# Kernel optimization log

Measured on AMD Instinct MI355X. Metric: run time of the kernel, lower is better.

The kernel has to match this reference:

```python
import jax, jax.numpy as jnp
import numpy as np
import math

S, E, D, H = 4096, 512, 64, 8  # sentence_length, imbd_size, hidden_size, num_heads


def setup_inputs() -> dict:
    key = jax.random.key(0)
    k1, k2, k3, k4, k5 = jax.random.split(key, 5)
    return {
        "X": jax.random.normal(k1, (S, E), dtype=jnp.float32),
        "W_q": jax.random.uniform(k2, (H, E, D), dtype=jnp.float32),
        "W_k": jax.random.uniform(k3, (H, E, D), dtype=jnp.float32),
        "W_v": jax.random.uniform(k4, (H, E, D), dtype=jnp.float32),
        "W_0": jax.random.uniform(k5, (E, D), dtype=jnp.float32),
    }


def reference(X, W_q, W_k, W_v, W_0):
    # Per-head projections: X [S,E] broadcast across heads -> [H,S,D]
    q = jnp.einsum('se,hed->hsd', X, W_q)
    k = jnp.einsum('se,hed->hsd', X, W_k)
    v = jnp.einsum('se,hed->hsd', X, W_v)
    # Scaled scores [H,S,S]; softmax over keys (last axis), no mask
    scores = jnp.einsum('hsd,htd->hst', q, k) / math.sqrt(D)
    attn = jax.nn.softmax(scores, axis=-1)
    r3 = jnp.einsum('hst,htd->hsd', attn, v)  # [H,S,D]
    # Concat heads: permute to [S,H,D] -> [S,H*D], then output proj [E,D]
    Z = r3.transpose(1, 0, 2).reshape(S, H * D) @ W_0  # [S,D]
    return Z
```

## Files before the change

kernel.cpp:

```cpp
#include <hip/hip_runtime.h>
#include <hip/hip_bf16.h>

#define S_LEN 4096
#define E_DIM 512
#define D_DIM 64
#define H_NUM 8
#define KSPLIT 4
#define NKT ((S_LEN / KSPLIT) / 64)
#define QSCALE 0.18033688011112042f

typedef short bf16x8 __attribute__((ext_vector_type(8)));
typedef float f32x4 __attribute__((ext_vector_type(4)));
typedef unsigned short u16x8 __attribute__((ext_vector_type(8)));
typedef unsigned short u16x4 __attribute__((ext_vector_type(4)));

__device__ inline unsigned short f2bf(float x) {
    union { float f; unsigned u; } v; v.f = x;
    unsigned r = v.u + 0x7FFFu + ((v.u >> 16) & 1u);
    return (unsigned short)(r >> 16);
}
__device__ inline float bf2f(unsigned short b) {
    union { unsigned u; float f; } v; v.u = ((unsigned)b) << 16;
    return v.f;
}
__device__ inline f32x4 mfma16(bf16x8 a, bf16x8 b, f32x4 c) {
    return __builtin_amdgcn_mfma_f32_16x16x32_bf16(a, b, c, 0, 0, 0);
}
__device__ inline void gl_lds16(const void* g, void* l) {
    __builtin_amdgcn_global_load_lds(
        (const __attribute__((address_space(1))) void*)g,
        (__attribute__((address_space(3))) void*)l, 16, 0, 0);
}
__device__ inline unsigned cvtpk(float a, float b) {
    unsigned r;
    asm volatile("v_cvt_pk_bf16_f32 %0, %1, %2" : "=v"(r) : "v"(a), "v"(b));
    return r;
}

__global__ __launch_bounds__(256) void prepass_x(
    const float* __restrict__ X, unsigned short* __restrict__ Xhi,
    unsigned short* __restrict__ Xlo)
{
    int i = (blockIdx.x * 256 + threadIdx.x) * 4;
    float4 v = *(const float4*)&X[i];
    float a[4] = {v.x, v.y, v.z, v.w};
    u16x4 hv, lv;
#pragma unroll
    for (int j = 0; j < 4; ++j) {
        unsigned short hb = f2bf(a[j]);
        hv[j] = hb;
        lv[j] = f2bf(a[j] - bf2f(hb));
    }
    *(u16x4*)&Xhi[i] = hv;
    *(u16x4*)&Xlo[i] = lv;
}

__global__ __launch_bounds__(256) void prepass_w(
    const float* __restrict__ Wq, const float* __restrict__ Wk,
    const float* __restrict__ Wv, unsigned short* __restrict__ WT)
{
    int z = blockIdx.y;
    const float* W = (z == 0) ? Wq : (z == 1) ? Wk : Wv;
    int idx = blockIdx.x * 256 + threadIdx.x;
    int n = idx >> 7;
    int e = (idx & 127) * 4;
    int hh = n >> 6, d = n & 63;
    unsigned short* Whi = WT + (size_t)z * 2 * 262144;
    unsigned short* Wlo = Whi + 262144;
    u16x4 hv, lv;
#pragma unroll
    for (int j = 0; j < 4; ++j) {
        float v = W[((size_t)hh * E_DIM + e + j) * D_DIM + d];
        unsigned short hb = f2bf(v);
        hv[j] = hb;
        lv[j] = f2bf(v - bf2f(hb));
    }
    *(u16x4*)&Whi[(size_t)n * E_DIM + e] = hv;
    *(u16x4*)&Wlo[(size_t)n * E_DIM + e] = lv;
}

__global__ __launch_bounds__(256) void proj_kernel(
    const unsigned short* __restrict__ Xhi, const unsigned short* __restrict__ Xlo,
    const unsigned short* __restrict__ WT,
    unsigned short* __restrict__ Qhi, unsigned short* __restrict__ Qlo,
    unsigned short* __restrict__ Khi, unsigned short* __restrict__ Klo,
    unsigned short* __restrict__ Vb)
{
    __shared__ __align__(16) unsigned short XhS[128 * 64];
    __shared__ __align__(16) unsigned short XlS[128 * 64];
    __shared__ __align__(16) unsigned short WhS[128 * 64];
    __shared__ __align__(16) unsigned short WlS[128 * 64];

    const int s0 = blockIdx.x * 128, n0 = blockIdx.y * 128, z = blockIdx.z;
    const unsigned short* Wh_g = WT + (size_t)z * 524288;
    const unsigned short* Wl_g = Wh_g + 262144;

    const int tid = threadIdx.x, lane = tid & 63, w = tid >> 6;
    const int l15 = lane & 15, lhi = lane >> 4;
    const int wr = w >> 1, wc = w & 1;

    const int chunk = lane & 7;
    size_t aoff[4], boff[4];
    int ldso[4];
#pragma unroll
    for (int i = 0; i < 4; ++i) {
        int r = w * 32 + i * 8 + (lane >> 3);
        int swz = (chunk * 16) ^ ((r & 7) << 4);
        aoff[i] = ((size_t)(s0 + r)) * 1024 + swz;
        boff[i] = ((size_t)(n0 + r)) * 1024 + swz;
        ldso[i] = (w * 32 + i * 8) * 128;
    }

    f32x4 acc[4][4];
#pragma unroll
    for (int a = 0; a < 4; ++a)
#pragma unroll
        for (int b = 0; b < 4; ++b) acc[a][b] = (f32x4){0.f, 0.f, 0.f, 0.f};

    for (int kb = 0; kb < E_DIM; kb += 64) {
        __syncthreads();
#pragma unroll
        for (int i = 0; i < 4; ++i) {
            size_t ab = aoff[i] + kb * 2;
            size_t bb = boff[i] + kb * 2;
            gl_lds16((const char*)Xhi + ab, (char*)XhS + ldso[i]);
            gl_lds16((const char*)Xlo + ab, (char*)XlS + ldso[i]);
            gl_lds16((const char*)Wh_g + bb, (char*)WhS + ldso[i]);
            gl_lds16((const char*)Wl_g + bb, (char*)WlS + ldso[i]);
        }
        __syncthreads();

#pragma unroll
        for (int kc = 0; kc < 2; ++kc) {
            int cb = kc * 64 + lhi * 16;
            bf16x8 ah[4], al[4], bh[4], bl[4];
#pragma unroll
            for (int rt = 0; rt < 4; ++rt) {
                int row = wr * 64 + rt * 16 + l15;
                int ad = row * 128 + (cb ^ ((row & 7) << 4));
                ah[rt] = *(const bf16x8*)((const char*)XhS + ad);
                al[rt] = *(const bf16x8*)((const char*)XlS + ad);
            }
#pragma unroll
            for (int nt = 0; nt < 4; ++nt) {
                int n = wc * 64 + nt * 16 + l15;
                int bd = n * 128 + (cb ^ ((n & 7) << 4));
                bh[nt] = *(const bf16x8*)((const char*)WhS + bd);
                bl[nt] = *(const bf16x8*)((const char*)WlS + bd);
            }
#pragma unroll
            for (int rt = 0; rt < 4; ++rt)
#pragma unroll
                for (int nt = 0; nt < 4; ++nt) {
                    acc[rt][nt] = mfma16(ah[rt], bh[nt], acc[rt][nt]);
                    acc[rt][nt] = mfma16(ah[rt], bl[nt], acc[rt][nt]);
                    acc[rt][nt] = mfma16(al[rt], bh[nt], acc[rt][nt]);
                }
        }
    }

#pragma unroll
    for (int rt = 0; rt < 4; ++rt)
#pragma unroll
        for (int nt = 0; nt < 4; ++nt) {
            int n = n0 + wc * 64 + nt * 16 + l15;
            int hh = n >> 6, d = n & 63;
#pragma unroll
            for (int j = 0; j < 4; ++j) {
                int s = s0 + wr * 64 + rt * 16 + lhi * 4 + j;
                float val = acc[rt][nt][j];
                size_t o = ((size_t)hh * S_LEN + s) * D_DIM + d;
                if (z == 0) {
                    val *= QSCALE;
                    unsigned short hb = f2bf(val);
                    Qhi[o] = hb;
                    Qlo[o] = f2bf(val - bf2f(hb));
                } else if (z == 1) {
                    unsigned short hb = f2bf(val);
                    Khi[o] = hb;
                    Klo[o] = f2bf(val - bf2f(hb));
                } else {
                    Vb[o] = f2bf(val);
                }
            }
        }
}

__global__ __launch_bounds__(256) void pack_vt(
    const unsigned short* __restrict__ Vb, unsigned short* __restrict__ Vt)
{
    __shared__ unsigned short T[64][72];
    int h = blockIdx.y, sblk = blockIdx.x * 64;
    int t = threadIdx.x;
#pragma unroll
    for (int p = 0; p < 2; ++p) {
        int slot = t + 256 * p;
        int s = slot >> 3, c = slot & 7;
        u16x8 v = *(const u16x8*)&Vb[((size_t)h * S_LEN + sblk + s) * D_DIM + c * 8];
#pragma unroll
        for (int j = 0; j < 8; ++j) T[c * 8 + j][s] = v[j];
    }
    __syncthreads();
#pragma unroll
    for (int p = 0; p < 2; ++p) {
        int slot = t + 256 * p;
        int d = slot >> 3, c = slot & 7;
        u16x8 v;
#pragma unroll
        for (int j = 0; j < 8; ++j) v[j] = T[d][c * 8 + j];
        *(u16x8*)&Vt[((size_t)(h * D_DIM + d)) * S_LEN + sblk + c * 8] = v;
    }
}

__global__ __launch_bounds__(256) void flash_kernel(
    const unsigned short* __restrict__ Qhi, const unsigned short* __restrict__ Qlo,
    const unsigned short* __restrict__ Khi_g, const unsigned short* __restrict__ Klo_g,
    const unsigned short* __restrict__ Vt_g,
    unsigned short* __restrict__ Part, float2* __restrict__ ML)
{
    __shared__ __align__(16) unsigned short KhiS[64 * 64];
    __shared__ __align__(16) unsigned short KloS[64 * 64];
    __shared__ __align__(16) unsigned short VtS[64 * 64];
    __shared__ __align__(16) unsigned short PS[4][16 * 64];

    const int h  = blockIdx.y;
    const int ks = blockIdx.z;
    const int q0 = blockIdx.x * 64;
    const int tid  = threadIdx.x;
    const int lane = tid & 63;
    const int w    = tid >> 6;
    const int l15  = lane & 15;
    const int lhi  = lane >> 4;

    const int qrow = q0 + w * 16 + l15;
    bf16x8 qh[2], ql[2];
#pragma unroll
    for (int c = 0; c < 2; ++c) {
        size_t off = ((size_t)(h * S_LEN + qrow)) * D_DIM + lhi * 8 + 32 * c;
        qh[c] = *(const bf16x8*)&Qhi[off];
        ql[c] = *(const bf16x8*)&Qlo[off];
    }

    const char *pKh[2], *pKl[2], *pV[2];
    int ldsd[2];
    {
        const int chunk = lane & 7;
#pragma unroll
        for (int i = 0; i < 2; ++i) {
            int r = w * 16 + i * 8 + (lane >> 3);
            int swz = (chunk * 16) ^ ((r & 7) << 4);
            size_t kb = ((size_t)(h * S_LEN + ks * (S_LEN / KSPLIT) + r)) * 128 + swz;
            pKh[i] = (const char*)Khi_g + kb;
            pKl[i] = (const char*)Klo_g + kb;
            size_t vb = ((size_t)(h * D_DIM + r) * S_LEN + ks * (S_LEN / KSPLIT)) * 2 + swz;
            pV[i] = (const char*)Vt_g + vb;
            ldsd[i] = (w * 16 + i * 8) * 128;
        }
    }

    f32x4 acc_o[4];
#pragma unroll
    for (int nt = 0; nt < 4; ++nt) acc_o[nt] = (f32x4){0.f, 0.f, 0.f, 0.f};
    float m2 = -1e30f, lsum = 0.f;

    unsigned short* pw = &PS[w][0];

    for (int kt = 0; kt < NKT; ++kt) {
        __syncthreads();
#pragma unroll
        for (int i = 0; i < 2; ++i) {
            gl_lds16(pKh[i], (char*)KhiS + ldsd[i]);
            gl_lds16(pKl[i], (char*)KloS + ldsd[i]);
            gl_lds16(pV[i],  (char*)VtS  + ldsd[i]);
            pKh[i] += 8192; pKl[i] += 8192; pV[i] += 128;
        }
        __syncthreads();

        f32x4 sacc[4];
#pragma unroll
        for (int nt = 0; nt < 4; ++nt) sacc[nt] = (f32x4){0.f, 0.f, 0.f, 0.f};
#pragma unroll
        for (int c = 0; c < 2; ++c) {
            int colb = (lhi * 8 + 32 * c) * 2;
#pragma unroll
            for (int nt = 0; nt < 4; ++nt) {
                int key = l15 + 16 * nt;
                int lo = key * 128 + (((colb >> 4) ^ (key & 7)) << 4);
                bf16x8 kh = *(const bf16x8*)((const char*)KhiS + lo);
                bf16x8 kl = *(const bf16x8*)((const char*)KloS + lo);
                sacc[nt] = mfma16(kh, qh[c], sacc[nt]);
                sacc[nt] = mfma16(kl, qh[c], sacc[nt]);
                sacc[nt] = mfma16(kh, ql[c], sacc[nt]);
            }
        }

        float mx0 = fmaxf(fmaxf(sacc[0][0], sacc[0][1]), fmaxf(sacc[0][2], sacc[0][3]));
        float mx1 = fmaxf(fmaxf(sacc[1][0], sacc[1][1]), fmaxf(sacc[1][2], sacc[1][3]));
        float mx2 = fmaxf(fmaxf(sacc[2][0], sacc[2][1]), fmaxf(sacc[2][2], sacc[2][3]));
        float mx3 = fmaxf(fmaxf(sacc[3][0], sacc[3][1]), fmaxf(sacc[3][2], sacc[3][3]));
        float vm = fmaxf(fmaxf(mx0, mx1), fmaxf(mx2, mx3));
        vm = fmaxf(vm, __shfl_xor(vm, 16));
        vm = fmaxf(vm, __shfl_xor(vm, 32));

        if (!__all(vm <= m2 + 8.f)) {
            float mnew = fmaxf(m2, vm);
            float sc = exp2f(m2 - mnew);
            m2 = mnew;
            lsum *= sc;
            float scj[4];
#pragma unroll
            for (int j = 0; j < 4; ++j) scj[j] = __shfl(sc, lhi * 4 + j);
#pragma unroll
            for (int nt = 0; nt < 4; ++nt)
#pragma unroll
                for (int j = 0; j < 4; ++j) acc_o[nt][j] *= scj[j];
        }

        float sum = 0.f;
#pragma unroll
        for (int nt = 0; nt < 4; ++nt) {
            float e0 = exp2f(sacc[nt][0] - m2);
            float e1 = exp2f(sacc[nt][1] - m2);
            float e2 = exp2f(sacc[nt][2] - m2);
            float e3 = exp2f(sacc[nt][3] - m2);
            sum += (e0 + e1) + (e2 + e3);
            int colb = 32 * nt + 8 * lhi;
            int adr = l15 * 128 + ((((colb >> 4)) ^ (l15 & 7)) << 4) + (colb & 15);
            uint2 pk = make_uint2(cvtpk(e0, e1), cvtpk(e2, e3));
            *(uint2*)((char*)pw + adr) = pk;
        }
        sum += __shfl_xor(sum, 16);
        sum += __shfl_xor(sum, 32);
        lsum += sum;

#pragma unroll
        for (int c = 0; c < 2; ++c) {
            int colb = (lhi * 8 + 32 * c) * 2;
            int loA = l15 * 128 + (((colb >> 4) ^ (l15 & 7)) << 4);
            bf16x8 pa = *(const bf16x8*)((const char*)pw + loA);
#pragma unroll
            for (int nt = 0; nt < 4; ++nt) {
                int d = l15 + 16 * nt;
                int loB = d * 128 + (((colb >> 4) ^ (d & 7)) << 4);
                bf16x8 vb = *(const bf16x8*)((const char*)VtS + loB);
                acc_o[nt] = mfma16(pa, vb, acc_o[nt]);
            }
        }
    }

    if (lane < 16) {
        ML[(size_t)(ks * H_NUM + h) * S_LEN + q0 + w * 16 + l15] =
            make_float2(m2, lsum);
    }
    unsigned short* PT = Part + ((size_t)(ks * H_NUM + h)) * S_LEN * D_DIM;
#pragma unroll
    for (int r = 0; r < 4; ++r) {
        float lr = __shfl(lsum, lhi * 4 + r);
        float inv = 1.f / lr;
        int s = q0 + w * 16 + lhi * 4 + r;
#pragma unroll
        for (int nt = 0; nt < 4; ++nt)
            PT[(size_t)s * D_DIM + l15 + 16 * nt] = f2bf(acc_o[nt][r] * inv);
    }
}

__global__ __launch_bounds__(256) void cw_kernel(
    const float2* __restrict__ ML, float4* __restrict__ CW)
{
    int i = blockIdx.x * 256 + threadIdx.x;
    float2 a[KSPLIT];
    float m = -1e30f;
#pragma unroll
    for (int k = 0; k < KSPLIT; ++k) {
        a[k] = ML[(size_t)k * H_NUM * S_LEN + i];
        m = fmaxf(m, a[k].x);
    }
    float wk[KSPLIT], wsum = 0.f;
#pragma unroll
    for (int k = 0; k < KSPLIT; ++k) {
        wk[k] = exp2f(a[k].x - m) * a[k].y;
        wsum += wk[k];
    }
    float inv = 1.f / wsum;
    CW[i] = make_float4(wk[0] * inv, wk[1] * inv, wk[2] * inv, wk[3] * inv);
}

__global__ __launch_bounds__(256) void zout_kernel(
    const unsigned short* __restrict__ Part, const float4* __restrict__ CW,
    const float* __restrict__ W0, float* __restrict__ Z)
{
    __shared__ __align__(16) float Rs[32][64];
    __shared__ __align__(16) float Ws[32][64];

    const size_t PSZ = (size_t)H_NUM * S_LEN * D_DIM;
    const int s0 = blockIdx.x * 64;
    const int tid = threadIdx.x;
    const int tx = tid & 15;
    const int ty = tid >> 4;

    float acc[4][4];
#pragma unroll
    for (int i = 0; i < 4; ++i)
#pragma unroll
        for (int j = 0; j < 4; ++j) acc[i][j] = 0.f;

    for (int kb = 0; kb < E_DIM; kb += 32) {
        __syncthreads();
#pragma unroll
        for (int p = 0; p < 2; ++p) {
            int idx = tid + 256 * p;
            int row = idx >> 3;
            int kq  = idx & 7;
            int k = kb + kq * 4;
            int hh = k >> 6, d0 = k & 63;
            int s = s0 + row;
            size_t pbase = ((size_t)hh * S_LEN + s) * D_DIM + d0;
            float4 c = *(const float4*)&CW[hh * S_LEN + s];
            u16x4 a0 = *(const u16x4*)&Part[pbase];
            u16x4 a1 = *(const u16x4*)&Part[PSZ + pbase];
            u16x4 a2 = *(const u16x4*)&Part[2 * PSZ + pbase];
            u16x4 a3 = *(const u16x4*)&Part[3 * PSZ + pbase];
#pragma unroll
            for (int j = 0; j < 4; ++j)
                Rs[kq * 4 + j][row] = bf2f(a0[j]) * c.x + bf2f(a1[j]) * c.y +
                                      bf2f(a2[j]) * c.z + bf2f(a3[j]) * c.w;
        }
#pragma unroll
        for (int p = 0; p < 2; ++p) {
            int idx = tid + 256 * p;
            int k  = idx >> 4;
            int nq = idx & 15;
            *(float4*)&Ws[k][nq * 4] = *(const float4*)&W0[(size_t)(kb + k) * D_DIM + nq * 4];
        }
        __syncthreads();

#pragma unroll 8
        for (int k = 0; k < 32; ++k) {
            float a[4], b[4];
            *(float4*)&a[0] = *(const float4*)&Rs[k][ty * 4];
            *(float4*)&b[0] = *(const float4*)&Ws[k][tx * 4];
#pragma unroll
            for (int i = 0; i < 4; ++i)
#pragma unroll
                for (int j = 0; j < 4; ++j) acc[i][j] += a[i] * b[j];
        }
    }

#pragma unroll
    for (int i = 0; i < 4; ++i) {
        float4 o = make_float4(acc[i][0], acc[i][1], acc[i][2], acc[i][3]);
        *(float4*)&Z[(size_t)(s0 + ty * 4 + i) * D_DIM + tx * 4] = o;
    }
}

extern "C" void kernel_launch(void* const* d_in, const int* in_sizes, int n_in,
                              void* d_out, int out_size, void* d_ws, size_t ws_size,
                              hipStream_t stream) {
    const float* X  = (const float*)d_in[0];
    const float* Wq = (const float*)d_in[1];
    const float* Wk = (const float*)d_in[2];
    const float* Wv = (const float*)d_in[3];
    const float* W0 = (const float*)d_in[4];

    char* ws = (char*)d_ws;
    const size_t MB = 1ull << 20;
    unsigned short* Qhi = (unsigned short*)(ws + 0 * MB);
    unsigned short* Qlo = (unsigned short*)(ws + 4 * MB);
    unsigned short* Khi = (unsigned short*)(ws + 8 * MB);
    unsigned short* Klo = (unsigned short*)(ws + 12 * MB);
    unsigned short* Vt  = (unsigned short*)(ws + 16 * MB);
    unsigned short* Vb  = (unsigned short*)(ws + 20 * MB);
    unsigned short* Xhi = (unsigned short*)(ws + 24 * MB);
    unsigned short* Xlo = (unsigned short*)(ws + 28 * MB);
    unsigned short* WT  = (unsigned short*)(ws + 32 * MB);
    unsigned short* Part = (unsigned short*)(ws + 20 * MB);
    float2* ML = (float2*)(ws + 36 * MB);
    float4* CW = (float4*)(ws + 37 * MB);

    float* Z = (float*)d_out;

    prepass_x<<<dim3(S_LEN * E_DIM / 4 / 256), 256, 0, stream>>>(X, Xhi, Xlo);
    prepass_w<<<dim3(E_DIM * 128 / 256, 3), 256, 0, stream>>>(Wq, Wk, Wv, WT);
    proj_kernel<<<dim3(S_LEN / 128, 4, 3), 256, 0, stream>>>(
        Xhi, Xlo, WT, Qhi, Qlo, Khi, Klo, Vb);
    pack_vt<<<dim3(S_LEN / 64, H_NUM), 256, 0, stream>>>(Vb, Vt);
    flash_kernel<<<dim3(S_LEN / 64, H_NUM, KSPLIT), 256, 0, stream>>>(
        Qhi, Qlo, Khi, Klo, Vt, Part, ML);
    cw_kernel<<<dim3(H_NUM * S_LEN / 256), 256, 0, stream>>>(ML, CW);
    zout_kernel<<<dim3(S_LEN / 64), 256, 0, stream>>>(Part, CW, W0, Z);
}
```

Measured before the change: 228.2 us.

## Double-buffer flash K/V tiles, fuse prepasses, write V transposed directly

```diff
diff --git a/kernel.cpp b/kernel.cpp
--- a/kernel.cpp
+++ b/kernel.cpp
@@ -37,46 +37,47 @@
     return r;
 }
 
-__global__ __launch_bounds__(256) void prepass_x(
-    const float* __restrict__ X, unsigned short* __restrict__ Xhi,
-    unsigned short* __restrict__ Xlo)
+__global__ __launch_bounds__(256) void prepass_kernel(
+    const float* __restrict__ X, const float* __restrict__ Wq,
+    const float* __restrict__ Wk, const float* __restrict__ Wv,
+    unsigned short* __restrict__ Xhi, unsigned short* __restrict__ Xlo,
+    unsigned short* __restrict__ WT)
 {
-    int i = (blockIdx.x * 256 + threadIdx.x) * 4;
-    float4 v = *(const float4*)&X[i];
-    float a[4] = {v.x, v.y, v.z, v.w};
-    u16x4 hv, lv;
-#pragma unroll
-    for (int j = 0; j < 4; ++j) {
-        unsigned short hb = f2bf(a[j]);
-        hv[j] = hb;
-        lv[j] = f2bf(a[j] - bf2f(hb));
-    }
-    *(u16x4*)&Xhi[i] = hv;
-    *(u16x4*)&Xlo[i] = lv;
-}
-
-__global__ __launch_bounds__(256) void prepass_w(
-    const float* __restrict__ Wq, const float* __restrict__ Wk,
-    const float* __restrict__ Wv, unsigned short* __restrict__ WT)
-{
-    int z = blockIdx.y;
-    const float* W = (z == 0) ? Wq : (z == 1) ? Wk : Wv;
-    int idx = blockIdx.x * 256 + threadIdx.x;
-    int n = idx >> 7;
-    int e = (idx & 127) * 4;
-    int hh = n >> 6, d = n & 63;
-    unsigned short* Whi = WT + (size_t)z * 2 * 262144;
-    unsigned short* Wlo = Whi + 262144;
-    u16x4 hv, lv;
-#pragma unroll
-    for (int j = 0; j < 4; ++j) {
-        float v = W[((size_t)hh * E_DIM + e + j) * D_DIM + d];
-        unsigned short hb = f2bf(v);
-        hv[j] = hb;
-        lv[j] = f2bf(v - bf2f(hb));
-    }
-    *(u16x4*)&Whi[(size_t)n * E_DIM + e] = hv;
-    *(u16x4*)&Wlo[(size_t)n * E_DIM + e] = lv;
+    int bx = blockIdx.x;
+    if (bx < 2048) {
+        int i = (bx * 256 + threadIdx.x) * 4;
+        float4 v = *(const float4*)&X[i];
+        float a[4] = {v.x, v.y, v.z, v.w};
+        u16x4 hv, lv;
+#pragma unroll
+        for (int j = 0; j < 4; ++j) {
+            unsigned short hb = f2bf(a[j]);
+            hv[j] = hb;
+            lv[j] = f2bf(a[j] - bf2f(hb));
+        }
+        *(u16x4*)&Xhi[i] = hv;
+        *(u16x4*)&Xlo[i] = lv;
+    } else {
+        int wid = bx - 2048;
+        int z = wid >> 8;
+        const float* W = (z == 0) ? Wq : (z == 1) ? Wk : Wv;
+        int idx = (wid & 255) * 256 + threadIdx.x;
+        int n = idx >> 7;
+        int e = (idx & 127) * 4;
+        int hh = n >> 6, d = n & 63;
+        unsigned short* Whi = WT + (size_t)z * 2 * 262144;
+        unsigned short* Wlo = Whi + 262144;
+        u16x4 hv, lv;
+#pragma unroll
+        for (int j = 0; j < 4; ++j) {
+            float v = W[((size_t)hh * E_DIM + e + j) * D_DIM + d];
+            unsigned short hb = f2bf(v);
+            hv[j] = hb;
+            lv[j] = f2bf(v - bf2f(hb));
+        }
+        *(u16x4*)&Whi[(size_t)n * E_DIM + e] = hv;
+        *(u16x4*)&Wlo[(size_t)n * E_DIM + e] = lv;
+    }
 }
 
 __global__ __launch_bounds__(256) void proj_kernel(
@@ -84,7 +85,7 @@
     const unsigned short* __restrict__ WT,
     unsigned short* __restrict__ Qhi, unsigned short* __restrict__ Qlo,
     unsigned short* __restrict__ Khi, unsigned short* __restrict__ Klo,
-    unsigned short* __restrict__ Vb)
+    unsigned short* __restrict__ Vt)
 {
     __shared__ __align__(16) unsigned short XhS[128 * 64];
     __shared__ __align__(16) unsigned short XlS[128 * 64];
@@ -165,51 +166,31 @@
         for (int nt = 0; nt < 4; ++nt) {
             int n = n0 + wc * 64 + nt * 16 + l15;
             int hh = n >> 6, d = n & 63;
-#pragma unroll
-            for (int j = 0; j < 4; ++j) {
-                int s = s0 + wr * 64 + rt * 16 + lhi * 4 + j;
-                float val = acc[rt][nt][j];
-                size_t o = ((size_t)hh * S_LEN + s) * D_DIM + d;
-                if (z == 0) {
-                    val *= QSCALE;
-                    unsigned short hb = f2bf(val);
-                    Qhi[o] = hb;
-                    Qlo[o] = f2bf(val - bf2f(hb));
-                } else if (z == 1) {
-                    unsigned short hb = f2bf(val);
-                    Khi[o] = hb;
-                    Klo[o] = f2bf(val - bf2f(hb));
-                } else {
-                    Vb[o] = f2bf(val);
+            if (z == 2) {
+                u16x4 vv;
+#pragma unroll
+                for (int j = 0; j < 4; ++j) vv[j] = f2bf(acc[rt][nt][j]);
+                int sb = s0 + wr * 64 + rt * 16 + lhi * 4;
+                *(u16x4*)&Vt[((size_t)(hh * D_DIM + d)) * S_LEN + sb] = vv;
+            } else {
+#pragma unroll
+                for (int j = 0; j < 4; ++j) {
+                    int s = s0 + wr * 64 + rt * 16 + lhi * 4 + j;
+                    float val = acc[rt][nt][j];
+                    size_t o = ((size_t)hh * S_LEN + s) * D_DIM + d;
+                    if (z == 0) {
+                        val *= QSCALE;
+                        unsigned short hb = f2bf(val);
+                        Qhi[o] = hb;
+                        Qlo[o] = f2bf(val - bf2f(hb));
+                    } else {
+                        unsigned short hb = f2bf(val);
+                        Khi[o] = hb;
+                        Klo[o] = f2bf(val - bf2f(hb));
+                    }
                 }
             }
         }
-}
-
-__global__ __launch_bounds__(256) void pack_vt(
-    const unsigned short* __restrict__ Vb, unsigned short* __restrict__ Vt)
-{
-    __shared__ unsigned short T[64][72];
-    int h = blockIdx.y, sblk = blockIdx.x * 64;
-    int t = threadIdx.x;
-#pragma unroll
-    for (int p = 0; p < 2; ++p) {
-        int slot = t + 256 * p;
-        int s = slot >> 3, c = slot & 7;
-        u16x8 v = *(const u16x8*)&Vb[((size_t)h * S_LEN + sblk + s) * D_DIM + c * 8];
-#pragma unroll
-        for (int j = 0; j < 8; ++j) T[c * 8 + j][s] = v[j];
-    }
-    __syncthreads();
-#pragma unroll
-    for (int p = 0; p < 2; ++p) {
-        int slot = t + 256 * p;
-        int d = slot >> 3, c = slot & 7;
-        u16x8 v;
-#pragma unroll
-        for (int j = 0; j < 8; ++j) v[j] = T[d][c * 8 + j];
-        *(u16x8*)&Vt[((size_t)(h * D_DIM + d)) * S_LEN + sblk + c * 8] = v;
-    }
 }
 
 __global__ __launch_bounds__(256) void flash_kernel(
@@ -218,9 +199,7 @@
     const unsigned short* __restrict__ Vt_g,
     unsigned short* __restrict__ Part, float2* __restrict__ ML)
 {
-    __shared__ __align__(16) unsigned short KhiS[64 * 64];
-    __shared__ __align__(16) unsigned short KloS[64 * 64];
-    __shared__ __align__(16) unsigned short VtS[64 * 64];
+    __shared__ __align__(16) char lds[2][24576];
     __shared__ __align__(16) unsigned short PS[4][16 * 64];
 
     const int h  = blockIdx.y;
@@ -258,6 +237,17 @@
         }
     }
 
+#define STAGE(B) do {                                            \
+        _Pragma("unroll")                                        \
+        for (int i = 0; i < 2; ++i) {                            \
+            char* base = &lds[(B)][0];                           \
+            gl_lds16(pKh[i], base + ldsd[i]);                    \
+            gl_lds16(pKl[i], base + 8192 + ldsd[i]);             \
+            gl_lds16(pV[i],  base + 16384 + ldsd[i]);            \
+            pKh[i] += 8192; pKl[i] += 8192; pV[i] += 128;        \
+        }                                                        \
+    } while (0)
+
     f32x4 acc_o[4];
 #pragma unroll
     for (int nt = 0; nt < 4; ++nt) acc_o[nt] = (f32x4){0.f, 0.f, 0.f, 0.f};
@@ -265,20 +255,21 @@
 
     unsigned short* pw = &PS[w][0];
 
+    STAGE(0);
+    __syncthreads();
+
+    int buf = 0;
     for (int kt = 0; kt < NKT; ++kt) {
-        __syncthreads();
-#pragma unroll
-        for (int i = 0; i < 2; ++i) {
-            gl_lds16(pKh[i], (char*)KhiS + ldsd[i]);
-            gl_lds16(pKl[i], (char*)KloS + ldsd[i]);
-            gl_lds16(pV[i],  (char*)VtS  + ldsd[i]);
-            pKh[i] += 8192; pKl[i] += 8192; pV[i] += 128;
-        }
-        __syncthreads();
+        if (kt + 1 < NKT) STAGE(buf ^ 1);
+
+        const char* Kh = &lds[buf][0];
+        const char* Kl = Kh + 8192;
+        const char* Vl = Kh + 16384;
 
         f32x4 sacc[4];
 #pragma unroll
         for (int nt = 0; nt < 4; ++nt) sacc[nt] = (f32x4){0.f, 0.f, 0.f, 0.f};
+        __builtin_amdgcn_s_setprio(1);
 #pragma unroll
         for (int c = 0; c < 2; ++c) {
             int colb = (lhi * 8 + 32 * c) * 2;
@@ -286,13 +277,14 @@
             for (int nt = 0; nt < 4; ++nt) {
                 int key = l15 + 16 * nt;
                 int lo = key * 128 + (((colb >> 4) ^ (key & 7)) << 4);
-                bf16x8 kh = *(const bf16x8*)((const char*)KhiS + lo);
-                bf16x8 kl = *(const bf16x8*)((const char*)KloS + lo);
+                bf16x8 kh = *(const bf16x8*)(Kh + lo);
+                bf16x8 kl = *(const bf16x8*)(Kl + lo);
                 sacc[nt] = mfma16(kh, qh[c], sacc[nt]);
                 sacc[nt] = mfma16(kl, qh[c], sacc[nt]);
                 sacc[nt] = mfma16(kh, ql[c], sacc[nt]);
             }
         }
+        __builtin_amdgcn_s_setprio(0);
 
         float mx0 = fmaxf(fmaxf(sacc[0][0], sacc[0][1]), fmaxf(sacc[0][2], sacc[0][3]));
         float mx1 = fmaxf(fmaxf(sacc[1][0], sacc[1][1]), fmaxf(sacc[1][2], sacc[1][3]));
@@ -333,6 +325,7 @@
         sum += __shfl_xor(sum, 32);
         lsum += sum;
 
+        __builtin_amdgcn_s_setprio(1);
 #pragma unroll
         for (int c = 0; c < 2; ++c) {
             int colb = (lhi * 8 + 32 * c) * 2;
@@ -342,11 +335,18 @@
             for (int nt = 0; nt < 4; ++nt) {
                 int d = l15 + 16 * nt;
                 int loB = d * 128 + (((colb >> 4) ^ (d & 7)) << 4);
-                bf16x8 vb = *(const bf16x8*)((const char*)VtS + loB);
+                bf16x8 vb = *(const bf16x8*)(Vl + loB);
                 acc_o[nt] = mfma16(pa, vb, acc_o[nt]);
             }
         }
-    }
+        __builtin_amdgcn_s_setprio(0);
+
+        if (kt + 1 < NKT) {
+            __syncthreads();
+            buf ^= 1;
+        }
+    }
+#undef STAGE
 
     if (lane < 16) {
         ML[(size_t)(ks * H_NUM + h) * S_LEN + q0 + w * 16 + l15] =
@@ -469,7 +469,6 @@
     unsigned short* Khi = (unsigned short*)(ws + 8 * MB);
     unsigned short* Klo = (unsigned short*)(ws + 12 * MB);
     unsigned short* Vt  = (unsigned short*)(ws + 16 * MB);
-    unsigned short* Vb  = (unsigned short*)(ws + 20 * MB);
     unsigned short* Xhi = (unsigned short*)(ws + 24 * MB);
     unsigned short* Xlo = (unsigned short*)(ws + 28 * MB);
     unsigned short* WT  = (unsigned short*)(ws + 32 * MB);
@@ -479,11 +478,9 @@
 
     float* Z = (float*)d_out;
 
-    prepass_x<<<dim3(S_LEN * E_DIM / 4 / 256), 256, 0, stream>>>(X, Xhi, Xlo);
-    prepass_w<<<dim3(E_DIM * 128 / 256, 3), 256, 0, stream>>>(Wq, Wk, Wv, WT);
+    prepass_kernel<<<dim3(2048 + 768), 256, 0, stream>>>(X, Wq, Wk, Wv, Xhi, Xlo, WT);
     proj_kernel<<<dim3(S_LEN / 128, 4, 3), 256, 0, stream>>>(
-        Xhi, Xlo, WT, Qhi, Qlo, Khi, Klo, Vb);
-    pack_vt<<<dim3(S_LEN / 64, H_NUM), 256, 0, stream>>>(Vb, Vt);
+        Xhi, Xlo, WT, Qhi, Qlo, Khi, Klo, Vt);
     flash_kernel<<<dim3(S_LEN / 64, H_NUM, KSPLIT), 256, 0, stream>>>(
         Qhi, Qlo, Khi, Klo, Vt, Part, ML);
     cw_kernel<<<dim3(H_NUM * S_LEN / 256), 256, 0, stream>>>(ML, CW);
```

New measurement: 246.7 us. 1.08x slower.
